# Kernel tuning notes

Measured on AMD Instinct MI355X. Metric: run time of the kernel, lower is better.

## Reference

```python
import jax, jax.numpy as jnp
import numpy as np

L, D, H, HID, V, MAXLEN = 4, 768, 12, 3072, 32000, 1024
HD = D // H

def _pe_table(max_len, d_model):
    pos = np.arange(max_len)[:, None].astype(np.float64)
    i = np.arange(d_model)[None, :]
    ang = pos / np.power(10000.0, 2 * (i // 2) / d_model)
    ang[:, 0::2] = np.sin(ang[:, 0::2])
    ang[:, 1::2] = np.cos(ang[:, 1::2])
    return jnp.asarray(ang, dtype=jnp.float32)

def _layernorm(x, g, b, eps=1e-5):
    mu = jnp.mean(x, axis=-1, keepdims=True)
    var = jnp.mean(jnp.square(x - mu), axis=-1, keepdims=True)
    return (x - mu) * jax.lax.rsqrt(var + eps) * g + b

def setup_inputs() -> dict:
    key = jax.random.key(0)
    ks = jax.random.split(key, 16)
    s = 0.02
    inp = {
        'tokens': jax.random.randint(ks[0], (4, 1024), 0, V),
        'emb': jax.random.normal(ks[1], (V, D), jnp.float32) * s,
        'pe': _pe_table(MAXLEN, D),
        'ln1_g': jnp.ones((L, D), jnp.float32), 'ln1_b': jnp.zeros((L, D), jnp.float32),
        'wq': jax.random.normal(ks[2], (L, D, D), jnp.float32) * s, 'bq': jnp.zeros((L, D), jnp.float32),
        'wk': jax.random.normal(ks[3], (L, D, D), jnp.float32) * s, 'bk': jnp.zeros((L, D), jnp.float32),
        'wv': jax.random.normal(ks[4], (L, D, D), jnp.float32) * s, 'bv': jnp.zeros((L, D), jnp.float32),
        'wo': jax.random.normal(ks[5], (L, D, D), jnp.float32) * s, 'bo': jnp.zeros((L, D), jnp.float32),
        'ln2_g': jnp.ones((L, D), jnp.float32), 'ln2_b': jnp.zeros((L, D), jnp.float32),
        'w1': jax.random.normal(ks[6], (L, D, HID), jnp.float32) * s, 'b1': jnp.zeros((L, HID), jnp.float32),
        'w2': jax.random.normal(ks[7], (L, HID, D), jnp.float32) * s, 'b2': jnp.zeros((L, D), jnp.float32),
        'lnf_g': jnp.ones((D,), jnp.float32), 'lnf_b': jnp.zeros((D,), jnp.float32),
        'w_out': jax.random.normal(ks[8], (D, V), jnp.float32) * s,
    }
    return inp

def reference(tokens, emb, pe, ln1_g, ln1_b, wq, bq, wk, bk, wv, bv, wo, bo, ln2_g, ln2_b, w1, b1, w2, b2, lnf_g, lnf_b, w_out):
    B, S = tokens.shape
    x = emb[tokens] + pe[:S]  # [B,S,D]
    causal = jnp.tril(jnp.ones((S, S), bool))  # True = keep
    scale = 1.0 / jnp.sqrt(jnp.float32(D))  # NOTE: module scales by sqrt(d_model), not sqrt(head_dim)
    for l in range(L):
        h = _layernorm(x, ln1_g[l], ln1_b[l])
        def heads(w, b):
            return (h @ w + b).reshape(B, S, H, HD).transpose(0, 2, 1, 3)  # [B,H,S,HD]
        q, k, v = heads(wq[l], bq[l]), heads(wk[l], bk[l]), heads(wv[l], bv[l])
        scores = jnp.einsum('bhqd,bhkd->bhqk', q, k) * scale
        scores = jnp.where(causal, scores, -jnp.inf)
        probs = jax.nn.softmax(scores, axis=-1)
        attn = jnp.einsum('bhqk,bhkd->bhqd', probs, v)
        attn = attn.transpose(0, 2, 1, 3).reshape(B, S, D)
        x = x + attn @ wo[l] + bo[l]
        h2 = _layernorm(x, ln2_g[l], ln2_b[l])
        x = x + jax.nn.relu(h2 @ w1[l] + b1[l]) @ w2[l] + b2[l]
    hs = _layernorm(x, lnf_g, lnf_b)
    return hs @ w_out  # [B,S,V]
```

## Files before the change

kernel.cpp:

```cpp
#include <hip/hip_runtime.h>


typedef __bf16 bf16_t;
typedef bf16_t bf16x8 __attribute__((ext_vector_type(8)));
typedef float f32x4 __attribute__((ext_vector_type(4)));

#define GLD16(G, L) __builtin_amdgcn_global_load_lds(                          \
    (const __attribute__((address_space(1))) unsigned int*)(const void*)(G),   \
    (__attribute__((address_space(3))) unsigned int*)(void*)(L), 16, 0, 0)

__device__ __forceinline__ f32x4 mfma16(bf16x8 a, bf16x8 b, f32x4 c) {
  return __builtin_amdgcn_mfma_f32_16x16x32_bf16(a, b, c, 0, 0, 0);
}

__device__ __forceinline__ void barrier_raw() {
  asm volatile("s_barrier" ::: "memory");
}

#define RED16_MAX(x) { x = fmaxf(x, __shfl_xor(x, 1)); x = fmaxf(x, __shfl_xor(x, 2)); \
                       x = fmaxf(x, __shfl_xor(x, 4)); x = fmaxf(x, __shfl_xor(x, 8)); }
#define RED16_SUM(x) { x += __shfl_xor(x, 1); x += __shfl_xor(x, 2); \
                       x += __shfl_xor(x, 4); x += __shfl_xor(x, 8); }

__device__ __forceinline__ int SW64(int row, int col) {
  return row * 64 + (col ^ ((row & 7) << 3));
}

__global__ __launch_bounds__(256)
void tconv_k(const float* __restrict__ in, bf16_t* __restrict__ out, int K, int N,
             size_t in_ls, size_t out_ls) {
  __shared__ float tile[32][33];
  in  += (size_t)blockIdx.z * in_ls;
  out += (size_t)blockIdx.z * out_ls;
  const int n0 = blockIdx.x * 32, k0 = blockIdx.y * 32;
  const int tx = threadIdx.x & 31, ty = threadIdx.x >> 5;
#pragma unroll
  for (int j = 0; j < 4; ++j)
    tile[ty + j * 8][tx] = in[(size_t)(k0 + ty + j * 8) * N + n0 + tx];
  __syncthreads();
#pragma unroll
  for (int j = 0; j < 4; ++j)
    out[(size_t)(n0 + ty + j * 8) * K + k0 + tx] = (bf16_t)tile[tx][ty + j * 8];
}

__global__ void qkvbias_k(const float* __restrict__ bq, const float* __restrict__ bk,
                          const float* __restrict__ bv, float* __restrict__ out) {
  const int l = blockIdx.x;
  for (int j = threadIdx.x; j < 2304; j += 256) {
    float v = (j < 768) ? bq[l * 768 + j]
            : (j < 1536) ? bk[l * 768 + j - 768]
                         : bv[l * 768 + j - 1536];
    out[l * 2304 + j] = v;
  }
}

__global__ __launch_bounds__(256)
void embed_k(const int* __restrict__ tok, const float* __restrict__ emb,
             const float* __restrict__ pe, float* __restrict__ xf) {
  const int row = blockIdx.x, tid = threadIdx.x;
  const int s = row & 1023;
  const int t = tok[row];
  float* o = xf + (size_t)row * 768;
  const float* e = emb + (size_t)t * 768;
  const float* p = pe + (size_t)s * 768;
  o[tid]       = e[tid]       + p[tid];
  o[tid + 256] = e[tid + 256] + p[tid + 256];
  o[tid + 512] = e[tid + 512] + p[tid + 512];
}

__global__ __launch_bounds__(256)
void ln_k(const float* __restrict__ x, const float* __restrict__ g,
          const float* __restrict__ bb, bf16_t* __restrict__ out) {
  const int row = blockIdx.x, tid = threadIdx.x;
  const int wave = tid >> 6, lane = tid & 63;
  const float* xr = x + (size_t)row * 768;
  float v0 = xr[tid], v1 = xr[tid + 256], v2 = xr[tid + 512];
  float s = v0 + v1 + v2;
  __shared__ float red[4];
#pragma unroll
  for (int off = 32; off; off >>= 1) s += __shfl_xor(s, off);
  if (lane == 0) red[wave] = s;
  __syncthreads();
  const float mu = (red[0] + red[1] + red[2] + red[3]) * (1.0f / 768.0f);
  const float d0 = v0 - mu, d1 = v1 - mu, d2 = v2 - mu;
  float s2 = d0 * d0 + d1 * d1 + d2 * d2;
#pragma unroll
  for (int off = 32; off; off >>= 1) s2 += __shfl_xor(s2, off);
  __syncthreads();
  if (lane == 0) red[wave] = s2;
  __syncthreads();
  const float rstd = rsqrtf((red[0] + red[1] + red[2] + red[3]) * (1.0f / 768.0f) + 1e-5f);
  bf16_t* orow = out + (size_t)row * 768;
  orow[tid]       = (bf16_t)(d0 * rstd * g[tid]       + bb[tid]);
  orow[tid + 256] = (bf16_t)(d1 * rstd * g[tid + 256] + bb[tid + 256]);
  orow[tid + 512] = (bf16_t)(d2 * rstd * g[tid + 512] + bb[tid + 512]);
}

template <bool BIAS, bool RELU, bool OUTF32, bool NT, int SUPER>
__global__ __launch_bounds__(512, 2)
void gemm8p(const bf16_t* __restrict__ A, const bf16_t* __restrict__ BT,
            const float* __restrict__ bias,
            float* __restrict__ outF, bf16_t* __restrict__ outB,
            int M, int N, int K) {
  extern __shared__ char smem[];
  const int NT_TILES = K >> 6;
  const int tilesM = M >> 8;
  const int cpx = gridDim.x >> 3;
  const int blk = ((int)blockIdx.x & 7) * cpx + ((int)blockIdx.x >> 3);
  int tm, tn;
  if (SUPER > 0) {
    const int grp = SUPER * tilesM;
    const int g = blk / grp, r = blk % grp;
    tm = r / SUPER;
    tn = g * SUPER + r % SUPER;
  } else {
    tm = blk % tilesM;
    tn = blk / tilesM;
  }
  const int tid = threadIdx.x;
  const int lane = tid & 63, wave = tid >> 6;
  const int wr = wave >> 2, wc = wave & 3;
  const int lrow = lane & 15, koct = lane >> 4;

  const size_t rowK = (size_t)K * 2;
  const int srow = tid >> 3;
  const int cswz = ((tid & 7) ^ (srow & 7)) << 4;
  const char* gA = (const char*)(A + (size_t)tm * 256 * K) + (size_t)srow * rowK + cswz;
  const char* gB = (const char*)(BT + (size_t)tn * 256 * K) + (size_t)srow * rowK + cswz;

  const int swz = (lrow & 7) << 4;
  const int aB0 = (wr * 128 + lrow) * 128 + ((koct * 16) ^ swz);
  const int bB0 = 32768 + (wc * 64 + lrow) * 128 + ((koct * 16) ^ swz);

  auto stageA = [&](int t) {
    char* d = smem + ((t & 1) << 16);
    const size_t kb = (size_t)t * 128;
    GLD16(gA + kb,              d + tid * 16);
    GLD16(gA + 64 * rowK + kb,  d + 8192 + tid * 16);
    GLD16(gA + 128 * rowK + kb, d + 16384 + tid * 16);
    GLD16(gA + 192 * rowK + kb, d + 24576 + tid * 16);
  };
  auto stageB = [&](int t) {
    char* d = smem + ((t & 1) << 16) + 32768;
    const size_t kb = (size_t)t * 128;
    GLD16(gB + kb,              d + tid * 16);
    GLD16(gB + 64 * rowK + kb,  d + 8192 + tid * 16);
    GLD16(gB + 128 * rowK + kb, d + 16384 + tid * 16);
    GLD16(gB + 192 * rowK + kb, d + 24576 + tid * 16);
  };

  stageA(0); stageB(0);
  stageA(1); stageB(1);

  f32x4 acc[8][4] = {};

  for (int t = 0; t < NT_TILES; ++t) {
    const char* rb = smem + ((t & 1) << 16);
    const bool pf = (t + 2) < NT_TILES;
    if (t == NT_TILES - 1) asm volatile("s_waitcnt vmcnt(0)" ::: "memory");
    else                   asm volatile("s_waitcnt vmcnt(8)" ::: "memory");
    barrier_raw();

    bf16x8 a0[4][2], a1[4][2], b[4][2];
#pragma unroll
    for (int mi = 0; mi < 4; ++mi) {
      const int o = aB0 + mi * 2048;
      a0[mi][0] = *(const bf16x8*)(rb + o);
      a0[mi][1] = *(const bf16x8*)(rb + (o ^ 64));
    }
#pragma unroll
    for (int ni = 0; ni < 2; ++ni) {
      const int o = bB0 + ni * 2048;
      b[ni][0] = *(const bf16x8*)(rb + o);
      b[ni][1] = *(const bf16x8*)(rb + (o ^ 64));
    }
    barrier_raw();
    __builtin_amdgcn_s_setprio(1);
#pragma unroll
    for (int mi = 0; mi < 4; ++mi)
#pragma unroll
      for (int ni = 0; ni < 2; ++ni) {
        acc[mi][ni] = mfma16(a0[mi][0], b[ni][0], acc[mi][ni]);
        acc[mi][ni] = mfma16(a0[mi][1], b[ni][1], acc[mi][ni]);
      }
    __builtin_amdgcn_s_setprio(0);
    barrier_raw();

#pragma unroll
    for (int ni = 2; ni < 4; ++ni) {
      const int o = bB0 + ni * 2048;
      b[ni][0] = *(const bf16x8*)(rb + o);
      b[ni][1] = *(const bf16x8*)(rb + (o ^ 64));
    }
    __builtin_amdgcn_s_setprio(1);
#pragma unroll
    for (int mi = 0; mi < 4; ++mi)
#pragma unroll
      for (int ni = 2; ni < 4; ++ni) {
        acc[mi][ni] = mfma16(a0[mi][0], b[ni][0], acc[mi][ni]);
        acc[mi][ni] = mfma16(a0[mi][1], b[ni][1], acc[mi][ni]);
      }
    __builtin_amdgcn_s_setprio(0);
    asm volatile("s_waitcnt lgkmcnt(0)" ::: "memory");
    barrier_raw();

    if (pf) stageB(t + 2);
#pragma unroll
    for (int mi = 0; mi < 4; ++mi) {
      const int o = aB0 + (mi + 4) * 2048;
      a1[mi][0] = *(const bf16x8*)(rb + o);
      a1[mi][1] = *(const bf16x8*)(rb + (o ^ 64));
    }
    __builtin_amdgcn_s_setprio(1);
#pragma unroll
    for (int mi = 0; mi < 4; ++mi)
#pragma unroll
      for (int ni = 0; ni < 2; ++ni) {
        acc[mi + 4][ni] = mfma16(a1[mi][0], b[ni][0], acc[mi + 4][ni]);
        acc[mi + 4][ni] = mfma16(a1[mi][1], b[ni][1], acc[mi + 4][ni]);
      }
    __builtin_amdgcn_s_setprio(0);
    asm volatile("s_waitcnt lgkmcnt(0)" ::: "memory");
    barrier_raw();

    if (pf) stageA(t + 2);
    __builtin_amdgcn_s_setprio(1);
#pragma unroll
    for (int mi = 0; mi < 4; ++mi)
#pragma unroll
      for (int ni = 2; ni < 4; ++ni) {
        acc[mi + 4][ni] = mfma16(a1[mi][0], b[ni][0], acc[mi + 4][ni]);
        acc[mi + 4][ni] = mfma16(a1[mi][1], b[ni][1], acc[mi + 4][ni]);
      }
    __builtin_amdgcn_s_setprio(0);
  }

  barrier_raw();
  const int row0 = tm * 256 + wr * 128, col0 = tn * 256 + wc * 64;
  float bv[4];
#pragma unroll
  for (int ni = 0; ni < 4; ++ni)
    bv[ni] = BIAS ? bias[col0 + ni * 16 + lrow] : 0.0f;

  if (OUTF32) {
    float* lf = (float*)smem + wave * (32 * 68);
#pragma unroll
    for (int ph = 0; ph < 4; ++ph) {
#pragma unroll
      for (int mm = 0; mm < 2; ++mm) {
        const int mi = ph * 2 + mm;
#pragma unroll
        for (int ni = 0; ni < 4; ++ni)
#pragma unroll
          for (int r = 0; r < 4; ++r) {
            float v = acc[mi][ni][r] + bv[ni];
            if (RELU) v = fmaxf(v, 0.0f);
            lf[(mm * 16 + koct * 4 + r) * 68 + ni * 16 + lrow] = v;
          }
      }
#pragma unroll
      for (int j = 0; j < 8; ++j) {
        const int lr = j * 4 + koct;
        const int lc = lrow * 4;
        f32x4 v4 = *(const f32x4*)&lf[lr * 68 + lc];
        f32x4* dst = (f32x4*)&outF[(size_t)(row0 + ph * 32 + lr) * N + col0 + lc];
        if (NT) __builtin_nontemporal_store(v4, dst);
        else    *dst = v4;
      }
    }
  } else {
    bf16_t* lb = (bf16_t*)smem + wave * (32 * 72);
#pragma unroll
    for (int ph = 0; ph < 4; ++ph) {
#pragma unroll
      for (int mm = 0; mm < 2; ++mm) {
        const int mi = ph * 2 + mm;
#pragma unroll
        for (int ni = 0; ni < 4; ++ni)
#pragma unroll
          for (int r = 0; r < 4; ++r) {
            float v = acc[mi][ni][r] + bv[ni];
            if (RELU) v = fmaxf(v, 0.0f);
            lb[(mm * 16 + koct * 4 + r) * 72 + ni * 16 + lrow] = (bf16_t)v;
          }
      }
#pragma unroll
      for (int j = 0; j < 4; ++j) {
        const int lr = j * 8 + (lane >> 3);
        const int lc = (lane & 7) * 8;
        bf16x8 v8 = *(const bf16x8*)&lb[lr * 72 + lc];
        *(bf16x8*)&outB[(size_t)(row0 + ph * 32 + lr) * N + col0 + lc] = v8;
      }
    }
  }
}

template <bool BIAS, bool RELU, bool RESID, bool OUTF32>
__global__ __launch_bounds__(256, 2)
void gemmS(const bf16_t* __restrict__ A, const bf16_t* __restrict__ BT,
           const float* __restrict__ bias, const float* __restrict__ resid,
           float* __restrict__ outF, bf16_t* __restrict__ outB,
           int M, int N, int K) {
  extern __shared__ char smem[];
  const int NT = K >> 6;
  const int tiles_n = N >> 7;
  const int tm = blockIdx.x / tiles_n, tn = blockIdx.x % tiles_n;
  const int tid = threadIdx.x;
  const int wave = tid >> 6, lane = tid & 63;
  const int wr = wave >> 1, wc = wave & 1;
  const int lrow = lane & 15, koct = lane >> 4;

  const char* gA[2];
  const char* gB[4];
  {
    const char* Ab = (const char*)(A + (size_t)tm * 64 * K);
    const char* Bb = (const char*)(BT + (size_t)tn * 128 * K);
#pragma unroll
    for (int i = 0; i < 2; ++i) {
      const int off = i * 4096 + tid * 16;
      const int row = off >> 7;
      const int src = off ^ ((row & 7) << 4);
      gA[i] = Ab + (size_t)row * (2 * K) + (src & 127);
    }
#pragma unroll
    for (int i = 0; i < 4; ++i) {
      const int off = i * 4096 + tid * 16;
      const int row = off >> 7;
      const int src = off ^ ((row & 7) << 4);
      gB[i] = Bb + (size_t)row * (2 * K) + (src & 127);
    }
  }

  int aoff[2][2], boff[2][4];
#pragma unroll
  for (int kk = 0; kk < 2; ++kk) {
#pragma unroll
    for (int mi = 0; mi < 2; ++mi) {
      const int row = wr * 32 + mi * 16 + lrow;
      aoff[kk][mi] = (row * 128 + kk * 64 + koct * 16) ^ ((lrow & 7) << 4);
    }
#pragma unroll
    for (int ni = 0; ni < 4; ++ni) {
      const int row = wc * 64 + ni * 16 + lrow;
      boff[kk][ni] = 8192 + ((row * 128 + kk * 64 + koct * 16) ^ ((lrow & 7) << 4));
    }
  }

#pragma unroll
  for (int t = 0; t < 2; ++t) {
    char* sb = smem + t * 24576;
    const size_t kb = (size_t)t * 128;
    GLD16(gA[0] + kb, sb + tid * 16);
    GLD16(gA[1] + kb, sb + 4096 + tid * 16);
    GLD16(gB[0] + kb, sb + 8192 + tid * 16);
    GLD16(gB[1] + kb, sb + 12288 + tid * 16);
    GLD16(gB[2] + kb, sb + 16384 + tid * 16);
    GLD16(gB[3] + kb, sb + 20480 + tid * 16);
  }

  f32x4 acc[2][4] = {};

  for (int t = 0; t < NT; ++t) {
    char* sb = smem + (t % 3) * 24576;
    char* sb2 = smem + ((t + 2) % 3) * 24576;
    const bool pf = (t + 2) < NT;
    const size_t kb2 = (size_t)(t + 2) * 128;

    if (t == NT - 1) asm volatile("s_waitcnt vmcnt(0)" ::: "memory");
    else             asm volatile("s_waitcnt vmcnt(6)" ::: "memory");
    barrier_raw();

#pragma unroll
    for (int kk = 0; kk < 2; ++kk) {
      bf16x8 af[2], bfr[4];
#pragma unroll
      for (int mi = 0; mi < 2; ++mi)
        af[mi] = *(const bf16x8*)(sb + aoff[kk][mi]);
#pragma unroll
      for (int ni = 0; ni < 4; ++ni)
        bfr[ni] = *(const bf16x8*)(sb + boff[kk][ni]);
      if (pf) {
        if (kk == 0) {
          GLD16(gA[0] + kb2, sb2 + tid * 16);
          GLD16(gA[1] + kb2, sb2 + 4096 + tid * 16);
          GLD16(gB[0] + kb2, sb2 + 8192 + tid * 16);
        } else {
          GLD16(gB[1] + kb2, sb2 + 12288 + tid * 16);
          GLD16(gB[2] + kb2, sb2 + 16384 + tid * 16);
          GLD16(gB[3] + kb2, sb2 + 20480 + tid * 16);
        }
      }
      barrier_raw();
      __builtin_amdgcn_s_setprio(1);
#pragma unroll
      for (int mi = 0; mi < 2; ++mi)
#pragma unroll
        for (int ni = 0; ni < 4; ++ni)
          acc[mi][ni] = mfma16(af[mi], bfr[ni], acc[mi][ni]);
      __builtin_amdgcn_s_setprio(0);
    }
  }

  const int row0 = tm * 64 + wr * 32, col0 = tn * 128 + wc * 64;
#pragma unroll
  for (int ni = 0; ni < 4; ++ni) {
    const int col = col0 + ni * 16 + lrow;
    const float bv = BIAS ? bias[col] : 0.0f;
#pragma unroll
    for (int mi = 0; mi < 2; ++mi) {
#pragma unroll
      for (int r = 0; r < 4; ++r) {
        const int row = row0 + mi * 16 + koct * 4 + r;
        float v = acc[mi][ni][r] + bv;
        if (RELU) v = fmaxf(v, 0.0f);
        const size_t idx = (size_t)row * N + col;
        if (RESID) v += resid[idx];
        if (OUTF32) outF[idx] = v;
        else        outB[idx] = (bf16_t)v;
      }
    }
  }
}

__global__ __launch_bounds__(256)
void attn_k(const bf16_t* __restrict__ qkv, bf16_t* __restrict__ ab) {
  __shared__ __align__(16) bf16_t Qs[64 * 64];
  __shared__ __align__(16) bf16_t Ks[64 * 64];
  __shared__ __align__(16) bf16_t Vt[64 * 64];
  __shared__ __align__(16) bf16_t Ps[4][16 * 64];
  const int qt = blockIdx.x, h = blockIdx.y, b = blockIdx.z;
  const int tid = threadIdx.x;
  const int wave = tid >> 6, lane = tid & 63;
  const int lrow = lane & 15, koct = lane >> 4;
  const float scale = 0.03608439182435161f;

  const size_t RS = 2304;
  const bf16_t* qbase = qkv + h * 64;
  const bf16_t* kbase = qkv + 768 + h * 64;
  const bf16_t* vbase = qkv + 1536 + h * 64;

  const int sr = tid >> 3;
  const int sc = (((tid & 7) ^ (sr & 7)) << 3);

  {
#pragma unroll
    for (int i = 0; i < 2; ++i)
      GLD16(qbase + (size_t)(b * 1024 + qt * 64 + i * 32 + sr) * RS + sc,
            Qs + i * 2048 + tid * 8);
  }
  __syncthreads();
  bf16x8 qf[2];
  qf[0] = *(const bf16x8*)&Qs[SW64(wave * 16 + lrow, koct * 8)];
  qf[1] = *(const bf16x8*)&Qs[SW64(wave * 16 + lrow, 32 + koct * 8)];

  float m_r[4], l_r[4];
  f32x4 o[4] = {};
#pragma unroll
  for (int r = 0; r < 4; ++r) { m_r[r] = -1e30f; l_r[r] = 0.0f; }

  for (int kt = 0; kt <= qt; ++kt) {
    __syncthreads();
    {
#pragma unroll
      for (int i = 0; i < 2; ++i)
        GLD16(kbase + (size_t)(b * 1024 + kt * 64 + i * 32 + sr) * RS + sc,
              Ks + i * 2048 + tid * 8);
    }
    {
      const int kvr = lane;
      const int d0 = wave * 16;
      const bf16_t* vr = vbase + (size_t)(b * 1024 + kt * 64 + kvr) * RS + d0;
      bf16x8 v0 = *(const bf16x8*)vr;
      bf16x8 v1 = *(const bf16x8*)(vr + 8);
#pragma unroll
      for (int j = 0; j < 8; ++j) {
        Vt[(d0 + j) * 64 + (kvr ^ (j << 3))]     = v0[j];
        Vt[(d0 + 8 + j) * 64 + (kvr ^ (j << 3))] = v1[j];
      }
    }
    __syncthreads();

    f32x4 s[4] = {};
#pragma unroll
    for (int ni = 0; ni < 4; ++ni) {
      bf16x8 kf0 = *(const bf16x8*)&Ks[SW64(ni * 16 + lrow, koct * 8)];
      bf16x8 kf1 = *(const bf16x8*)&Ks[SW64(ni * 16 + lrow, 32 + koct * 8)];
      s[ni] = mfma16(qf[0], kf0, s[ni]);
      s[ni] = mfma16(qf[1], kf1, s[ni]);
    }

    const int qrow = qt * 64 + wave * 16 + koct * 4;
    float rm[4];
#pragma unroll
    for (int r = 0; r < 4; ++r) rm[r] = -1e30f;
#pragma unroll
    for (int ni = 0; ni < 4; ++ni) {
      const int kcol = kt * 64 + ni * 16 + lrow;
#pragma unroll
      for (int r = 0; r < 4; ++r) {
        float v = s[ni][r] * scale;
        if (kcol > qrow + r) v = -1e30f;
        s[ni][r] = v;
        rm[r] = fmaxf(rm[r], v);
      }
    }
#pragma unroll
    for (int r = 0; r < 4; ++r) RED16_MAX(rm[r]);
    float corr[4], ps[4];
#pragma unroll
    for (int r = 0; r < 4; ++r) {
      const float mn = fmaxf(m_r[r], rm[r]);
      corr[r] = __expf(m_r[r] - mn);
      m_r[r] = mn;
      ps[r] = 0.0f;
    }
#pragma unroll
    for (int ni = 0; ni < 4; ++ni)
#pragma unroll
      for (int r = 0; r < 4; ++r) {
        const float p = __expf(s[ni][r] - m_r[r]);
        s[ni][r] = p;
        ps[r] += p;
      }
#pragma unroll
    for (int r = 0; r < 4; ++r) RED16_SUM(ps[r]);
#pragma unroll
    for (int r = 0; r < 4; ++r) l_r[r] = l_r[r] * corr[r] + ps[r];
#pragma unroll
    for (int ni = 0; ni < 4; ++ni)
#pragma unroll
      for (int r = 0; r < 4; ++r) o[ni][r] *= corr[r];

#pragma unroll
    for (int ni = 0; ni < 4; ++ni)
#pragma unroll
      for (int r = 0; r < 4; ++r) {
        const int prow = koct * 4 + r;
        Ps[wave][prow * 64 + ((ni * 16 + lrow) ^ ((prow & 7) << 3))] =
            (bf16_t)s[ni][r];
      }
    __syncthreads();

    bf16x8 pa0 = *(const bf16x8*)&Ps[wave][SW64(lrow, koct * 8)];
    bf16x8 pa1 = *(const bf16x8*)&Ps[wave][SW64(lrow, 32 + koct * 8)];
#pragma unroll
    for (int ni = 0; ni < 4; ++ni) {
      bf16x8 vf0 = *(const bf16x8*)&Vt[SW64(ni * 16 + lrow, koct * 8)];
      bf16x8 vf1 = *(const bf16x8*)&Vt[SW64(ni * 16 + lrow, 32 + koct * 8)];
      o[ni] = mfma16(pa0, vf0, o[ni]);
      o[ni] = mfma16(pa1, vf1, o[ni]);
    }
  }

#pragma unroll
  for (int r = 0; r < 4; ++r) {
    const float inv = 1.0f / l_r[r];
    const int row = qt * 64 + wave * 16 + koct * 4 + r;
#pragma unroll
    for (int ni = 0; ni < 4; ++ni)
      ab[(size_t)(b * 1024 + row) * 768 + h * 64 + ni * 16 + lrow] =
          (bf16_t)(o[ni][r] * inv);
  }
}

extern "C" void kernel_launch(void* const* d_in, const int* in_sizes, int n_in,
                              void* d_out, int out_size, void* d_ws, size_t ws_size,
                              hipStream_t stream) {
  (void)in_sizes; (void)n_in; (void)out_size; (void)ws_size;
  const int*   tok   = (const int*)d_in[0];
  const float* emb   = (const float*)d_in[1];
  const float* pe    = (const float*)d_in[2];
  const float* ln1_g = (const float*)d_in[3];
  const float* ln1_b = (const float*)d_in[4];
  const float* wq    = (const float*)d_in[5];
  const float* bq    = (const float*)d_in[6];
  const float* wk    = (const float*)d_in[7];
  const float* bk    = (const float*)d_in[8];
  const float* wv    = (const float*)d_in[9];
  const float* bv    = (const float*)d_in[10];
  const float* wo    = (const float*)d_in[11];
  const float* bo    = (const float*)d_in[12];
  const float* ln2_g = (const float*)d_in[13];
  const float* ln2_b = (const float*)d_in[14];
  const float* w1    = (const float*)d_in[15];
  const float* b1    = (const float*)d_in[16];
  const float* w2    = (const float*)d_in[17];
  const float* b2    = (const float*)d_in[18];
  const float* lnf_g = (const float*)d_in[19];
  const float* lnf_b = (const float*)d_in[20];
  const float* w_out = (const float*)d_in[21];
  float* out = (float*)d_out;

  char* ws = (char*)d_ws;
  size_t off = 0;
  auto alloc = [&](size_t bytes) -> void* {
    void* p = ws + off;
    off += (bytes + 255) & ~(size_t)255;
    return p;
  };
  float*  xf      = (float*)alloc(4096ull * 768 * 4);
  bf16_t* hb      = (bf16_t*)alloc(4096ull * 768 * 2);
  bf16_t* qkvb    = (bf16_t*)alloc(4096ull * 2304 * 2);
  bf16_t* ab      = (bf16_t*)alloc(4096ull * 768 * 2);
  bf16_t* fb      = (bf16_t*)alloc(4096ull * 3072 * 2);
  float*  qkvbias = (float*)alloc(4ull * 2304 * 4);
  bf16_t* wqkvT   = (bf16_t*)alloc(4ull * 2304 * 768 * 2);
  bf16_t* woT     = (bf16_t*)alloc(4ull * 768 * 768 * 2);
  bf16_t* w1T     = (bf16_t*)alloc(4ull * 3072 * 768 * 2);
  bf16_t* w2T     = (bf16_t*)alloc(4ull * 768 * 3072 * 2);
  bf16_t* woutT   = (bf16_t*)alloc(32000ull * 768 * 2);

  tconv_k<<<dim3(24, 24, 4), 256, 0, stream>>>(wq, wqkvT, 768, 768,
      768ull * 768, 2304ull * 768);
  tconv_k<<<dim3(24, 24, 4), 256, 0, stream>>>(wk, wqkvT + 768ull * 768, 768, 768,
      768ull * 768, 2304ull * 768);
  tconv_k<<<dim3(24, 24, 4), 256, 0, stream>>>(wv, wqkvT + 2ull * 768 * 768, 768, 768,
      768ull * 768, 2304ull * 768);
  tconv_k<<<dim3(24, 24, 4), 256, 0, stream>>>(wo, woT, 768, 768,
      768ull * 768, 768ull * 768);
  tconv_k<<<dim3(96, 24, 4), 256, 0, stream>>>(w1, w1T, 768, 3072,
      768ull * 3072, 3072ull * 768);
  tconv_k<<<dim3(24, 96, 4), 256, 0, stream>>>(w2, w2T, 3072, 768,
      3072ull * 768, 768ull * 3072);
  tconv_k<<<dim3(1000, 24, 1), 256, 0, stream>>>(w_out, woutT, 768, 32000, 0, 0);
  qkvbias_k<<<4, 256, 0, stream>>>(bq, bk, bv, qkvbias);

  embed_k<<<4096, 256, 0, stream>>>(tok, emb, pe, xf);

  const size_t SMEM8P = 131072;
  const size_t SMEMS  = 3 * 24576;
  for (int l = 0; l < 4; ++l) {
    ln_k<<<4096, 256, 0, stream>>>(xf, ln1_g + l * 768, ln1_b + l * 768, hb);
    gemm8p<true, false, false, false, 0><<<16 * 9, 512, SMEM8P, stream>>>(
        hb, wqkvT + (size_t)l * 2304 * 768, qkvbias + l * 2304,
        nullptr, qkvb, 4096, 2304, 768);
    attn_k<<<dim3(16, 12, 4), 256, 0, stream>>>(qkvb, ab);
    gemmS<true, false, true, true><<<64 * 6, 256, SMEMS, stream>>>(
        ab, woT + (size_t)l * 768 * 768, bo + l * 768,
        xf, xf, nullptr, 4096, 768, 768);
    ln_k<<<4096, 256, 0, stream>>>(xf, ln2_g + l * 768, ln2_b + l * 768, hb);
    gemm8p<true, true, false, false, 0><<<16 * 12, 512, SMEM8P, stream>>>(
        hb, w1T + (size_t)l * 3072 * 768, b1 + l * 3072,
        nullptr, fb, 4096, 3072, 768);
    gemmS<true, false, true, true><<<64 * 6, 256, SMEMS, stream>>>(
        fb, w2T + (size_t)l * 768 * 3072, b2 + l * 768,
        xf, xf, nullptr, 4096, 768, 3072);
  }
  ln_k<<<4096, 256, 0, stream>>>(xf, lnf_g, lnf_b, hb);
  gemm8p<false, false, true, true, 5><<<16 * 125, 512, SMEM8P, stream>>>(
      hb, woutT, nullptr, out, nullptr, 4096, 32000, 768);
}
```

Measured before the change: 984.5 us.

## Add 128x128-tile GEMM for QKV/FFN1 and one-row-per-wave vectorized layernorm

Adds a new gemm128 kernel with 128x128 tiles, a double-buffered LDS ring and 8 waves, used for the QKV and FFN1 projections in place of the 256-tile gemm8p. The smaller tiles give 576 and 768 blocks instead of 144 and 192, filling the 256 CUs better and allowing more resident blocks. The layernorm now handles one row per wave with float4 loads and no shared-memory reduction or block barriers. In exchange, smaller tiles reuse each loaded operand less and issue more global traffic per FLOP.

```diff
diff --git a/kernel.cpp b/kernel.cpp
--- a/kernel.cpp
+++ b/kernel.cpp
@@ -3,6 +3,7 @@
 
 typedef __bf16 bf16_t;
 typedef bf16_t bf16x8 __attribute__((ext_vector_type(8)));
+typedef bf16_t bf16x4 __attribute__((ext_vector_type(4)));
 typedef float f32x4 __attribute__((ext_vector_type(4)));
 
 #define GLD16(G, L) __builtin_amdgcn_global_load_lds(                          \
@@ -71,29 +72,42 @@
 __global__ __launch_bounds__(256)
 void ln_k(const float* __restrict__ x, const float* __restrict__ g,
           const float* __restrict__ bb, bf16_t* __restrict__ out) {
-  const int row = blockIdx.x, tid = threadIdx.x;
-  const int wave = tid >> 6, lane = tid & 63;
+  const int wave = threadIdx.x >> 6, lane = threadIdx.x & 63;
+  const int row = blockIdx.x * 4 + wave;
   const float* xr = x + (size_t)row * 768;
-  float v0 = xr[tid], v1 = xr[tid + 256], v2 = xr[tid + 512];
-  float s = v0 + v1 + v2;
-  __shared__ float red[4];
+  f32x4 v[3];
+#pragma unroll
+  for (int c = 0; c < 3; ++c) v[c] = *(const f32x4*)&xr[c * 256 + lane * 4];
+  float s = 0.0f;
+#pragma unroll
+  for (int c = 0; c < 3; ++c)
+#pragma unroll
+    for (int i = 0; i < 4; ++i) s += v[c][i];
 #pragma unroll
   for (int off = 32; off; off >>= 1) s += __shfl_xor(s, off);
-  if (lane == 0) red[wave] = s;
-  __syncthreads();
-  const float mu = (red[0] + red[1] + red[2] + red[3]) * (1.0f / 768.0f);
-  const float d0 = v0 - mu, d1 = v1 - mu, d2 = v2 - mu;
-  float s2 = d0 * d0 + d1 * d1 + d2 * d2;
+  const float mu = s * (1.0f / 768.0f);
+  float s2 = 0.0f;
+#pragma unroll
+  for (int c = 0; c < 3; ++c)
+#pragma unroll
+    for (int i = 0; i < 4; ++i) {
+      const float d = v[c][i] - mu;
+      s2 += d * d;
+    }
 #pragma unroll
   for (int off = 32; off; off >>= 1) s2 += __shfl_xor(s2, off);
-  __syncthreads();
-  if (lane == 0) red[wave] = s2;
-  __syncthreads();
-  const float rstd = rsqrtf((red[0] + red[1] + red[2] + red[3]) * (1.0f / 768.0f) + 1e-5f);
+  const float rstd = rsqrtf(s2 * (1.0f / 768.0f) + 1e-5f);
   bf16_t* orow = out + (size_t)row * 768;
-  orow[tid]       = (bf16_t)(d0 * rstd * g[tid]       + bb[tid]);
-  orow[tid + 256] = (bf16_t)(d1 * rstd * g[tid + 256] + bb[tid + 256]);
-  orow[tid + 512] = (bf16_t)(d2 * rstd * g[tid + 512] + bb[tid + 512]);
+#pragma unroll
+  for (int c = 0; c < 3; ++c) {
+    const f32x4 gv = *(const f32x4*)&g[c * 256 + lane * 4];
+    const f32x4 bv = *(const f32x4*)&bb[c * 256 + lane * 4];
+    bf16x4 o;
+#pragma unroll
+    for (int i = 0; i < 4; ++i)
+      o[i] = (bf16_t)((v[c][i] - mu) * rstd * gv[i] + bv[i]);
+    *(bf16x4*)&orow[c * 256 + lane * 4] = o;
+  }
 }
 
 template <bool BIAS, bool RELU, bool OUTF32, bool NT, int SUPER>
@@ -292,6 +306,105 @@
         *(bf16x8*)&outB[(size_t)(row0 + ph * 32 + lr) * N + col0 + lc] = v8;
       }
     }
+  }
+}
+
+template <bool BIAS, bool RELU>
+__global__ __launch_bounds__(512, 4)
+void gemm128(const bf16_t* __restrict__ A, const bf16_t* __restrict__ BT,
+             const float* __restrict__ bias, bf16_t* __restrict__ outB,
+             int M, int N, int K) {
+  extern __shared__ char smem[];
+  const int NT_TILES = K >> 6;
+  const int tilesM = M >> 7;
+  const int cpx = gridDim.x >> 3;
+  const int blk = ((int)blockIdx.x & 7) * cpx + ((int)blockIdx.x >> 3);
+  const int tm = blk % tilesM, tn = blk / tilesM;
+  const int tid = threadIdx.x;
+  const int lane = tid & 63, wave = tid >> 6;
+  const int wr = wave >> 2, wc = wave & 3;
+  const int lrow = lane & 15, koct = lane >> 4;
+
+  const size_t rowK = (size_t)K * 2;
+  const int srow = tid >> 3;
+  const int cswz = ((tid & 7) ^ (srow & 7)) << 4;
+  const char* gA = (const char*)(A + (size_t)tm * 128 * K) + (size_t)srow * rowK + cswz;
+  const char* gB = (const char*)(BT + (size_t)tn * 128 * K) + (size_t)srow * rowK + cswz;
+
+  const int swz = (lrow & 7) << 4;
+  const int aB0 = (wr * 64 + lrow) * 128 + ((koct * 16) ^ swz);
+  const int bB0 = 16384 + (wc * 32 + lrow) * 128 + ((koct * 16) ^ swz);
+
+  auto stage = [&](int t) {
+    char* d = smem + ((t & 1) << 15);
+    const size_t kb = (size_t)t * 128;
+    GLD16(gA + kb,             d + tid * 16);
+    GLD16(gA + 64 * rowK + kb, d + 8192 + tid * 16);
+    GLD16(gB + kb,             d + 16384 + tid * 16);
+    GLD16(gB + 64 * rowK + kb, d + 24576 + tid * 16);
+  };
+
+  stage(0); stage(1);
+
+  f32x4 acc[4][2] = {};
+
+  for (int t = 0; t < NT_TILES; ++t) {
+    const char* rb = smem + ((t & 1) << 15);
+    const bool pf = (t + 2) < NT_TILES;
+    if (t == NT_TILES - 1) asm volatile("s_waitcnt vmcnt(0)" ::: "memory");
+    else                   asm volatile("s_waitcnt vmcnt(4)" ::: "memory");
+    barrier_raw();
+
+    bf16x8 a[4], b[2], a2[4], b2[2];
+#pragma unroll
+    for (int mi = 0; mi < 4; ++mi) a[mi] = *(const bf16x8*)(rb + aB0 + mi * 2048);
+#pragma unroll
+    for (int ni = 0; ni < 2; ++ni) b[ni] = *(const bf16x8*)(rb + bB0 + ni * 2048);
+    barrier_raw();
+    __builtin_amdgcn_s_setprio(1);
+#pragma unroll
+    for (int mi = 0; mi < 4; ++mi)
+#pragma unroll
+      for (int ni = 0; ni < 2; ++ni)
+        acc[mi][ni] = mfma16(a[mi], b[ni], acc[mi][ni]);
+    __builtin_amdgcn_s_setprio(0);
+
+#pragma unroll
+    for (int mi = 0; mi < 4; ++mi) a2[mi] = *(const bf16x8*)(rb + ((aB0 + mi * 2048) ^ 64));
+#pragma unroll
+    for (int ni = 0; ni < 2; ++ni) b2[ni] = *(const bf16x8*)(rb + ((bB0 + ni * 2048) ^ 64));
+    __builtin_amdgcn_s_setprio(1);
+#pragma unroll
+    for (int mi = 0; mi < 4; ++mi)
+#pragma unroll
+      for (int ni = 0; ni < 2; ++ni)
+        acc[mi][ni] = mfma16(a2[mi], b2[ni], acc[mi][ni]);
+    __builtin_amdgcn_s_setprio(0);
+    asm volatile("s_waitcnt lgkmcnt(0)" ::: "memory");
+    barrier_raw();
+    if (pf) stage(t + 2);
+  }
+
+  const int row0 = tm * 128 + wr * 64, col0 = tn * 128 + wc * 32;
+  bf16_t* lb = (bf16_t*)smem + wave * (64 * 36);
+#pragma unroll
+  for (int ni = 0; ni < 2; ++ni) {
+    const float bv = BIAS ? bias[col0 + ni * 16 + lrow] : 0.0f;
+#pragma unroll
+    for (int mi = 0; mi < 4; ++mi)
+#pragma unroll
+      for (int r = 0; r < 4; ++r) {
+        float v = acc[mi][ni][r] + bv;
+        if (RELU) v = fmaxf(v, 0.0f);
+        lb[(mi * 16 + koct * 4 + r) * 36 + ni * 16 + lrow] = (bf16_t)v;
+      }
+  }
+#pragma unroll
+  for (int j = 0; j < 4; ++j) {
+    const int lr = j * 16 + (lane >> 2);
+    const int lc = (lane & 3) * 8;
+    bf16x8 v8 = *(const bf16x8*)&lb[lr * 36 + lc];
+    *(bf16x8*)&outB[(size_t)(row0 + lr) * N + col0 + lc] = v8;
   }
 }
 
@@ -627,26 +740,27 @@
 
   embed_k<<<4096, 256, 0, stream>>>(tok, emb, pe, xf);
 
-  const size_t SMEM8P = 131072;
-  const size_t SMEMS  = 3 * 24576;
+  const size_t SMEM8P  = 131072;
+  const size_t SMEM128 = 65536;
+  const size_t SMEMS   = 3 * 24576;
   for (int l = 0; l < 4; ++l) {
-    ln_k<<<4096, 256, 0, stream>>>(xf, ln1_g + l * 768, ln1_b + l * 768, hb);
-    gemm8p<true, false, false, false, 0><<<16 * 9, 512, SMEM8P, stream>>>(
+    ln_k<<<1024, 256, 0, stream>>>(xf, ln1_g + l * 768, ln1_b + l * 768, hb);
+    gemm128<true, false><<<32 * 18, 512, SMEM128, stream>>>(
         hb, wqkvT + (size_t)l * 2304 * 768, qkvbias + l * 2304,
-        nullptr, qkvb, 4096, 2304, 768);
+        qkvb, 4096, 2304, 768);
     attn_k<<<dim3(16, 12, 4), 256, 0, stream>>>(qkvb, ab);
     gemmS<true, false, true, true><<<64 * 6, 256, SMEMS, stream>>>(
         ab, woT + (size_t)l * 768 * 768, bo + l * 768,
         xf, xf, nullptr, 4096, 768, 768);
-    ln_k<<<4096, 256, 0, stream>>>(xf, ln2_g + l * 768, ln2_b + l * 768, hb);
-    gemm8p<true, true, false, false, 0><<<16 * 12, 512, SMEM8P, stream>>>(
+    ln_k<<<1024, 256, 0, stream>>>(xf, ln2_g + l * 768, ln2_b + l * 768, hb);
+    gemm128<true, true><<<32 * 24, 512, SMEM128, stream>>>(
         hb, w1T + (size_t)l * 3072 * 768, b1 + l * 3072,
-        nullptr, fb, 4096, 3072, 768);
+        fb, 4096, 3072, 768);
     gemmS<true, false, true, true><<<64 * 6, 256, SMEMS, stream>>>(
         fb, w2T + (size_t)l * 768 * 3072, b2 + l * 768,
         xf, xf, nullptr, 4096, 768, 3072);
   }
-  ln_k<<<4096, 256, 0, stream>>>(xf, lnf_g, lnf_b, hb);
+  ln_k<<<1024, 256, 0, stream>>>(xf, lnf_g, lnf_b, hb);
   gemm8p<false, false, true, true, 5><<<16 * 125, 512, SMEM8P, stream>>>(
       hb, woutT, nullptr, out, nullptr, 4096, 32000, 768);
 }
```

New measurement: 1.048 ms. 6.5% more time.

## Use one wave per row in layernorm and restructure GEMM barrier schedule

Applied to the files above, without the earlier changes.

LayerNorm now assigns one wavefront per row with float4 loads and bf16x4 stores, which removes the shared-memory reductions and block-level __syncthreads; the grid shrinks to 1024 blocks accordingly. In the gemm8p main loop, barriers and LDS waits are repositioned so that each MFMA phase is preceded by a barrier plus lgkmcnt(0), and a barrier is added after the A prefetch. The extra barriers may add synchronisation stalls in the GEMM. They are meant to align LDS read completion with the compute phases.

```diff
diff --git a/kernel.cpp b/kernel.cpp
--- a/kernel.cpp
+++ b/kernel.cpp
@@ -3,6 +3,7 @@
 
 typedef __bf16 bf16_t;
 typedef bf16_t bf16x8 __attribute__((ext_vector_type(8)));
+typedef bf16_t bf16x4 __attribute__((ext_vector_type(4)));
 typedef float f32x4 __attribute__((ext_vector_type(4)));
 
 #define GLD16(G, L) __builtin_amdgcn_global_load_lds(                          \
@@ -15,6 +16,10 @@
 
 __device__ __forceinline__ void barrier_raw() {
   asm volatile("s_barrier" ::: "memory");
+}
+
+__device__ __forceinline__ void lgkm0() {
+  asm volatile("s_waitcnt lgkmcnt(0)" ::: "memory");
 }
 
 #define RED16_MAX(x) { x = fmaxf(x, __shfl_xor(x, 1)); x = fmaxf(x, __shfl_xor(x, 2)); \
@@ -71,29 +76,42 @@
 __global__ __launch_bounds__(256)
 void ln_k(const float* __restrict__ x, const float* __restrict__ g,
           const float* __restrict__ bb, bf16_t* __restrict__ out) {
-  const int row = blockIdx.x, tid = threadIdx.x;
-  const int wave = tid >> 6, lane = tid & 63;
+  const int wave = threadIdx.x >> 6, lane = threadIdx.x & 63;
+  const int row = blockIdx.x * 4 + wave;
   const float* xr = x + (size_t)row * 768;
-  float v0 = xr[tid], v1 = xr[tid + 256], v2 = xr[tid + 512];
-  float s = v0 + v1 + v2;
-  __shared__ float red[4];
+  f32x4 v[3];
+#pragma unroll
+  for (int c = 0; c < 3; ++c) v[c] = *(const f32x4*)&xr[c * 256 + lane * 4];
+  float s = 0.0f;
+#pragma unroll
+  for (int c = 0; c < 3; ++c)
+#pragma unroll
+    for (int i = 0; i < 4; ++i) s += v[c][i];
 #pragma unroll
   for (int off = 32; off; off >>= 1) s += __shfl_xor(s, off);
-  if (lane == 0) red[wave] = s;
-  __syncthreads();
-  const float mu = (red[0] + red[1] + red[2] + red[3]) * (1.0f / 768.0f);
-  const float d0 = v0 - mu, d1 = v1 - mu, d2 = v2 - mu;
-  float s2 = d0 * d0 + d1 * d1 + d2 * d2;
+  const float mu = s * (1.0f / 768.0f);
+  float s2 = 0.0f;
+#pragma unroll
+  for (int c = 0; c < 3; ++c)
+#pragma unroll
+    for (int i = 0; i < 4; ++i) {
+      const float d = v[c][i] - mu;
+      s2 += d * d;
+    }
 #pragma unroll
   for (int off = 32; off; off >>= 1) s2 += __shfl_xor(s2, off);
-  __syncthreads();
-  if (lane == 0) red[wave] = s2;
-  __syncthreads();
-  const float rstd = rsqrtf((red[0] + red[1] + red[2] + red[3]) * (1.0f / 768.0f) + 1e-5f);
+  const float rstd = rsqrtf(s2 * (1.0f / 768.0f) + 1e-5f);
   bf16_t* orow = out + (size_t)row * 768;
-  orow[tid]       = (bf16_t)(d0 * rstd * g[tid]       + bb[tid]);
-  orow[tid + 256] = (bf16_t)(d1 * rstd * g[tid + 256] + bb[tid + 256]);
-  orow[tid + 512] = (bf16_t)(d2 * rstd * g[tid + 512] + bb[tid + 512]);
+#pragma unroll
+  for (int c = 0; c < 3; ++c) {
+    const f32x4 gv = *(const f32x4*)&g[c * 256 + lane * 4];
+    const f32x4 bv = *(const f32x4*)&bb[c * 256 + lane * 4];
+    bf16x4 o;
+#pragma unroll
+    for (int i = 0; i < 4; ++i)
+      o[i] = (bf16_t)((v[c][i] - mu) * rstd * gv[i] + bv[i]);
+    *(bf16x4*)&orow[c * 256 + lane * 4] = o;
+  }
 }
 
 template <bool BIAS, bool RELU, bool OUTF32, bool NT, int SUPER>
@@ -175,6 +193,7 @@
       b[ni][1] = *(const bf16x8*)(rb + (o ^ 64));
     }
     barrier_raw();
+    lgkm0();
     __builtin_amdgcn_s_setprio(1);
 #pragma unroll
     for (int mi = 0; mi < 4; ++mi)
@@ -192,6 +211,8 @@
       b[ni][0] = *(const bf16x8*)(rb + o);
       b[ni][1] = *(const bf16x8*)(rb + (o ^ 64));
     }
+    barrier_raw();
+    lgkm0();
     __builtin_amdgcn_s_setprio(1);
 #pragma unroll
     for (int mi = 0; mi < 4; ++mi)
@@ -201,7 +222,6 @@
         acc[mi][ni] = mfma16(a0[mi][1], b[ni][1], acc[mi][ni]);
       }
     __builtin_amdgcn_s_setprio(0);
-    asm volatile("s_waitcnt lgkmcnt(0)" ::: "memory");
     barrier_raw();
 
     if (pf) stageB(t + 2);
@@ -211,6 +231,8 @@
       a1[mi][0] = *(const bf16x8*)(rb + o);
       a1[mi][1] = *(const bf16x8*)(rb + (o ^ 64));
     }
+    barrier_raw();
+    lgkm0();
     __builtin_amdgcn_s_setprio(1);
 #pragma unroll
     for (int mi = 0; mi < 4; ++mi)
@@ -220,10 +242,10 @@
         acc[mi + 4][ni] = mfma16(a1[mi][1], b[ni][1], acc[mi + 4][ni]);
       }
     __builtin_amdgcn_s_setprio(0);
-    asm volatile("s_waitcnt lgkmcnt(0)" ::: "memory");
     barrier_raw();
 
     if (pf) stageA(t + 2);
+    barrier_raw();
     __builtin_amdgcn_s_setprio(1);
 #pragma unroll
     for (int mi = 0; mi < 4; ++mi)
@@ -630,7 +652,7 @@
   const size_t SMEM8P = 131072;
   const size_t SMEMS  = 3 * 24576;
   for (int l = 0; l < 4; ++l) {
-    ln_k<<<4096, 256, 0, stream>>>(xf, ln1_g + l * 768, ln1_b + l * 768, hb);
+    ln_k<<<1024, 256, 0, stream>>>(xf, ln1_g + l * 768, ln1_b + l * 768, hb);
     gemm8p<true, false, false, false, 0><<<16 * 9, 512, SMEM8P, stream>>>(
         hb, wqkvT + (size_t)l * 2304 * 768, qkvbias + l * 2304,
         nullptr, qkvb, 4096, 2304, 768);
@@ -638,7 +660,7 @@
     gemmS<true, false, true, true><<<64 * 6, 256, SMEMS, stream>>>(
         ab, woT + (size_t)l * 768 * 768, bo + l * 768,
         xf, xf, nullptr, 4096, 768, 768);
-    ln_k<<<4096, 256, 0, stream>>>(xf, ln2_g + l * 768, ln2_b + l * 768, hb);
+    ln_k<<<1024, 256, 0, stream>>>(xf, ln2_g + l * 768, ln2_b + l * 768, hb);
     gemm8p<true, true, false, false, 0><<<16 * 12, 512, SMEM8P, stream>>>(
         hb, w1T + (size_t)l * 3072 * 768, b1 + l * 3072,
         nullptr, fb, 4096, 3072, 768);
@@ -646,7 +668,7 @@
         fb, w2T + (size_t)l * 768 * 3072, b2 + l * 768,
         xf, xf, nullptr, 4096, 768, 3072);
   }
-  ln_k<<<4096, 256, 0, stream>>>(xf, lnf_g, lnf_b, hb);
+  ln_k<<<1024, 256, 0, stream>>>(xf, lnf_g, lnf_b, hb);
   gemm8p<false, false, true, true, 5><<<16 * 125, 512, SMEM8P, stream>>>(
       hb, woutT, nullptr, out, nullptr, 4096, 32000, 768);
 }
```

New measurement: 992.0 us. No clear change (+0.8%).
